# Kernel optimization log

Measured on AMD Instinct MI355X. Metric: run time of the kernel, lower is better.

The kernel has to match this reference:

```python
import jax, jax.numpy as jnp
import numpy as np
from math import sqrt

D_MODEL = 1024
N_HEADS = 16
FFN = 4096
B, N = 2, 2048
EPS = 1e-5


def _layernorm(x, g, b):
    mu = jnp.mean(x, -1, keepdims=True)
    var = jnp.mean((x - mu) ** 2, -1, keepdims=True)
    return (x - mu) * jax.lax.rsqrt(var + EPS) * g + b


def setup_inputs() -> dict:
    key = jax.random.key(0)
    ks = jax.random.split(key, 12)
    s = 1.0 / sqrt(D_MODEL)
    sf = 1.0 / sqrt(FFN)
    inp = {
        "tgt": jax.random.normal(ks[0], (B, N, D_MODEL), jnp.float32),
        # True = masked. Causal: query i may attend to keys j <= i.
        "tgt_mask": jnp.triu(jnp.ones((N, N), jnp.bool_), k=1),
        "tgt_key_pad_mask": jnp.zeros((B, N), jnp.bool_),
        "Wq": jax.random.uniform(ks[1], (D_MODEL, D_MODEL), jnp.float32, -s, s),
        "Wk": jax.random.uniform(ks[2], (D_MODEL, D_MODEL), jnp.float32, -s, s),
        "Wv": jax.random.uniform(ks[3], (D_MODEL, D_MODEL), jnp.float32, -s, s),
        "Wo": jax.random.uniform(ks[4], (D_MODEL, D_MODEL), jnp.float32, -s, s),
        "bo": jax.random.uniform(ks[5], (D_MODEL,), jnp.float32, -s, s),
        "W1": jax.random.uniform(ks[6], (FFN, D_MODEL), jnp.float32, -s, s),
        "b1": jax.random.uniform(ks[7], (FFN,), jnp.float32, -s, s),
        "W2": jax.random.uniform(ks[8], (D_MODEL, FFN), jnp.float32, -sf, sf),
        "b2": jax.random.uniform(ks[9], (D_MODEL,), jnp.float32, -sf, sf),
        "g1": jnp.ones((D_MODEL,), jnp.float32),
        "beta1": jnp.zeros((D_MODEL,), jnp.float32),
        "g2": jnp.ones((D_MODEL,), jnp.float32),
        "beta2": jnp.zeros((D_MODEL,), jnp.float32),
    }
    return inp


def _mha(x, tgt_mask, pad_mask, Wq, Wk, Wv, Wo, bo):
    b, n, d = x.shape
    dk = d // N_HEADS
    q = (x @ Wq.T).reshape(b, n, N_HEADS, dk).transpose(0, 2, 1, 3)  # bhnd
    k = (x @ Wk.T).reshape(b, n, N_HEADS, dk).transpose(0, 2, 1, 3)
    v = (x @ Wv.T).reshape(b, n, N_HEADS, dk).transpose(0, 2, 1, 3)
    scores = jnp.einsum("bhqd,bhkd->bhqk", q, k) / sqrt(dk)
    mask = tgt_mask[None, None, :, :] | pad_mask[:, None, None, :]
    scores = jnp.where(mask, -jnp.inf, scores)
    att = jax.nn.softmax(scores, axis=-1)
    out = jnp.einsum("bhqk,bhkd->bhqd", att, v).transpose(0, 2, 1, 3).reshape(b, n, d)
    return out @ Wo.T + bo


def reference(tgt, tgt_mask, tgt_key_pad_mask, Wq, Wk, Wv, Wo, bo,
              W1, b1, W2, b2, g1, beta1, g2, beta2):
    # PostNorm logic (pre_norm=False), dropout=0 (eval)
    h = _mha(tgt, tgt_mask, tgt_key_pad_mask, Wq, Wk, Wv, Wo, bo)
    x = _layernorm(tgt + h, g1, beta1)
    m = jax.nn.gelu(x @ W1.T + b1, approximate=True) @ W2.T + b2
    return _layernorm(x + m, g2, beta2)
```

## Files before the change

### kernel.cpp

```cpp
#include <hip/hip_runtime.h>


#define DEV __device__ __forceinline__

typedef __attribute__((ext_vector_type(4)))  float f32x4;
typedef __attribute__((ext_vector_type(16))) float f32x16;
typedef __attribute__((ext_vector_type(8)))  short s16x8;

static constexpr int Bb   = 2;
static constexpr int NN   = 2048;
static constexpr int DM   = 1024;
static constexpr int HH   = 16;
static constexpr int DK   = 64;
static constexpr int FF   = 4096;
static constexpr int ROWS = Bb * NN;

#define AS1(p) ((const __attribute__((address_space(1))) void*)(p))
#define AS3(p) ((__attribute__((address_space(3))) void*)(p))

DEV unsigned short f2bf(float f) {
  unsigned u = __float_as_uint(f);
  u += 0x7fff + ((u >> 16) & 1);
  return (unsigned short)(u >> 16);
}
DEV float fexp2(float x) {
  float r;
  asm("v_exp_f32 %0, %1" : "=v"(r) : "v"(x));
  return r;
}
DEV unsigned cvtpk(float lo, float hi) {
  unsigned r;
  asm("v_cvt_pk_bf16_f32 %0, %1, %2" : "=v"(r) : "v"(lo), "v"(hi));
  return r;
}

__global__ __launch_bounds__(256) void k_cast7(
    const float* __restrict__ tgt, const float* __restrict__ Wq,
    const float* __restrict__ Wk, const float* __restrict__ Wv,
    const float* __restrict__ Wo, const float* __restrict__ W1,
    const float* __restrict__ W2,
    ushort* __restrict__ xb, ushort* __restrict__ wqb,
    ushort* __restrict__ w1b, ushort* __restrict__ w2b) {
  const int i = blockIdx.x * 256 + threadIdx.x;
  constexpr int S0 = 1048576;
  constexpr int S1 = 262144;
  const float4* src;
  ushort* dstp;
  if (i < S0)               { src = (const float4*)tgt + i;            dstp = xb  + (size_t)i * 4; }
  else if (i < S0 + S1)     { src = (const float4*)Wq + (i - S0);      dstp = wqb + (size_t)(i - S0) * 4; }
  else if (i < S0 + 2 * S1) { src = (const float4*)Wk + (i - S0 - S1); dstp = wqb + (size_t)(i - S0) * 4; }
  else if (i < S0 + 3 * S1) { src = (const float4*)Wv + (i - S0 - 2 * S1); dstp = wqb + (size_t)(i - S0) * 4; }
  else if (i < S0 + 4 * S1) { src = (const float4*)Wo + (i - S0 - 3 * S1); dstp = wqb + (size_t)(i - S0) * 4; }
  else if (i < 3 * S0)      { src = (const float4*)W1 + (i - 2 * S0);  dstp = w1b + (size_t)(i - 2 * S0) * 4; }
  else                      { src = (const float4*)W2 + (i - 3 * S0);  dstp = w2b + (size_t)(i - 3 * S0) * 4; }
  float4 v = *src;
  ushort4 o;
  o.x = f2bf(v.x); o.y = f2bf(v.y); o.z = f2bf(v.z); o.w = f2bf(v.w);
  *reinterpret_cast<ushort4*>(dstp) = o;
}

template <int EPI, int BN, bool QKV>
__global__ __launch_bounds__(256) void k_gemm(
    const ushort* __restrict__ A, const ushort* __restrict__ Bt,
    const float* __restrict__ bias, const float* __restrict__ resid,
    ushort* __restrict__ Cb, float* __restrict__ Cf,
    int K, int nbx) {
  __shared__ ushort As[2][128][32];
  __shared__ ushort Bs[2][BN][32];

  const int t = threadIdx.x;
  const int lane = t & 63, w = t >> 6;
  const int lr = lane & 15, lg = lane >> 4;
  const int lrow = lane >> 2, lc8 = (lane & 3) * 8;

  const int nwg = gridDim.x;
  const int bid = blockIdx.x;
  const int q8 = nwg >> 3, r8 = nwg & 7;
  const int xcd = bid & 7, lin = bid >> 3;
  const int wg = (xcd < r8 ? xcd * (q8 + 1) : r8 * (q8 + 1) + (xcd - r8) * q8) + lin;
  const int band = wg / (4 * nbx);
  const int inn  = wg % (4 * nbx);
  const int by = band * 4 + (inn & 3);
  const int bx = inn >> 2;

  const int bRow = by * 128;
  const int bCol = bx * BN;

  constexpr int NW = BN / 32;
  const int wRow = (w >> 1) * 64, wCol = (w & 1) * (BN / 2);

  const f32x4 zero = {0.f, 0.f, 0.f, 0.f};
  f32x4 acc[4][NW];
#pragma unroll
  for (int m = 0; m < 4; ++m)
#pragma unroll
    for (int n = 0; n < NW; ++n) acc[m][n] = zero;

  auto stage = [&](int buf, int kt) {
#pragma unroll
    for (int i = 0; i < 2; ++i) {
      int rr = w * 32 + i * 16;
      __builtin_amdgcn_global_load_lds(
          AS1(A + (size_t)(bRow + rr + lrow) * K + kt + lc8),
          AS3(&As[buf][rr][0]), 16, 0, 0);
    }
#pragma unroll
    for (int i = 0; i < BN / 64; ++i) {
      int rr = w * (BN / 4) + i * 16;
      __builtin_amdgcn_global_load_lds(
          AS1(Bt + (size_t)(bCol + rr + lrow) * K + kt + lc8),
          AS3(&Bs[buf][rr][0]), 16, 0, 0);
    }
  };

  stage(0, 0);
  const int nk = K / 32;
  for (int tt = 0; tt < nk; ++tt) {
    const int cur = tt & 1;
    __syncthreads();
    if (tt + 1 < nk) stage(cur ^ 1, (tt + 1) * 32);

    s16x8 af[4], bfr[NW];
#pragma unroll
    for (int m = 0; m < 4; ++m)
      af[m] = *reinterpret_cast<const s16x8*>(&As[cur][wRow + m * 16 + lr][lg * 8]);
#pragma unroll
    for (int n = 0; n < NW; ++n)
      bfr[n] = *reinterpret_cast<const s16x8*>(&Bs[cur][wCol + n * 16 + lr][lg * 8]);
#pragma unroll
    for (int m = 0; m < 4; ++m)
#pragma unroll
      for (int n = 0; n < NW; ++n)
        acc[m][n] = __builtin_amdgcn_mfma_f32_16x16x32_bf16(af[m], bfr[n], acc[m][n], 0, 0, 0);
  }

  ushort* CbOut = Cb;
  int colBase = bCol, Ncols = nbx * BN, third = 0;
  if (QKV) {
    third = bCol >> 10;
    CbOut = Cb + (size_t)third * ROWS * DM;
    colBase = bCol & 1023;
    Ncols = DM;
  }
#pragma unroll
  for (int m = 0; m < 4; ++m) {
    int gr = bRow + wRow + m * 16 + lg * 4;
#pragma unroll
    for (int n = 0; n < NW; ++n) {
      int gc = colBase + wCol + n * 16 + lr;
      float bv = (EPI == 1 || EPI == 2) ? bias[gc] : 0.0f;
#pragma unroll
      for (int r = 0; r < 4; ++r) {
        int nr = gr + r;
        float v = acc[m][n][r] + bv;
        if (EPI == 2) {
          size_t idx = (size_t)nr * Ncols + gc;
          Cf[idx] = v + resid[idx];
        } else if (EPI == 1) {
          size_t idx = (size_t)nr * Ncols + gc;
          float u = v + 0.044715f * v * v * v;
          float g = v / (1.0f + __expf(-1.5957691216057308f * u));
          CbOut[idx] = f2bf(g);
        } else {
          int gcs = gc;
          if (QKV && third == 1)
            gcs = (gc & ~63) | ((gc ^ ((nr & 7) << 3)) & 63);
          CbOut[(size_t)nr * Ncols + gcs] = f2bf(v);
        }
      }
    }
  }
}

__global__ __launch_bounds__(256) void k_vt(const ushort* __restrict__ V,
                                            ushort* __restrict__ vT) {
  __shared__ ushort Ls[64][72];
  const int t = threadIdx.x;
  const int n0 = blockIdx.x * 64;
  const int bh = blockIdx.y;
  const int b = bh >> 4, h = bh & 15;
  const int n = t >> 2;
#pragma unroll
  for (int half = 0; half < 2; ++half) {
    int c8 = ((t & 3) + half * 4) * 8;
    int4 v = *reinterpret_cast<const int4*>(
        V + ((size_t)(b * NN + n0 + n)) * DM + h * DK + c8);
    *reinterpret_cast<int4*>(&Ls[n][c8]) = v;
  }
  __syncthreads();
  const int d = t >> 2;
#pragma unroll
  for (int half = 0; half < 2; ++half) {
    int c = (t & 3) + half * 4;
    ushort tmp[8];
#pragma unroll
    for (int j = 0; j < 8; ++j) tmp[j] = Ls[c * 8 + j][d];
    size_t out = ((size_t)bh * DK + d) * NN + n0 + ((c ^ (d & 7)) * 8);
    *reinterpret_cast<int4*>(vT + out) = *reinterpret_cast<const int4*>(tmp);
  }
}

template <int WB>
__global__ __launch_bounds__(256) void k_ln(const float* __restrict__ in,
                                            const float* __restrict__ g,
                                            const float* __restrict__ bta,
                                            float* __restrict__ outf,
                                            ushort* __restrict__ outb) {
  const int row = blockIdx.x;
  const int t = threadIdx.x;
  float4 v = reinterpret_cast<const float4*>(in + (size_t)row * DM)[t];
  float s1 = v.x + v.y + v.z + v.w;
  float s2 = v.x * v.x + v.y * v.y + v.z * v.z + v.w * v.w;
#pragma unroll
  for (int m = 32; m; m >>= 1) {
    s1 += __shfl_xor(s1, m, 64);
    s2 += __shfl_xor(s2, m, 64);
  }
  __shared__ float red[2][4];
  if ((t & 63) == 0) { red[0][t >> 6] = s1; red[1][t >> 6] = s2; }
  __syncthreads();
  s1 = red[0][0] + red[0][1] + red[0][2] + red[0][3];
  s2 = red[1][0] + red[1][1] + red[1][2] + red[1][3];
  const float mu = s1 * (1.0f / DM);
  const float var = s2 * (1.0f / DM) - mu * mu;
  const float rstd = rsqrtf(var + 1e-5f);
  float4 gv = reinterpret_cast<const float4*>(g)[t];
  float4 bv = reinterpret_cast<const float4*>(bta)[t];
  float4 o;
  o.x = (v.x - mu) * rstd * gv.x + bv.x;
  o.y = (v.y - mu) * rstd * gv.y + bv.y;
  o.z = (v.z - mu) * rstd * gv.z + bv.z;
  o.w = (v.w - mu) * rstd * gv.w + bv.w;
  reinterpret_cast<float4*>(outf + (size_t)row * DM)[t] = o;
  if (WB) {
    ushort4 ob;
    ob.x = f2bf(o.x); ob.y = f2bf(o.y); ob.z = f2bf(o.z); ob.w = f2bf(o.w);
    reinterpret_cast<ushort4*>(outb + (size_t)row * DM)[t] = ob;
  }
}

static __device__ const unsigned char SCHED24[24][2] = {
  {15,0},{15,1},{7,2},
  {14,0},{14,1},{13,0},{13,1},{6,2},
  {12,0},{12,1},{11,0},{11,1},{5,2},
  {10,0},{10,1},{9,0},{9,1},{4,2},
  {8,0},{8,1},{3,2},{2,2},{1,2},{0,2}};

__global__ __launch_bounds__(256) void k_attn(const ushort* __restrict__ Q,
                                              const ushort* __restrict__ Kb,
                                              const ushort* __restrict__ vT,
                                              ushort* __restrict__ O,
                                              float* __restrict__ Op,
                                              float* __restrict__ ml) {
  __shared__ ushort Ks[2][64 * 64];
  __shared__ ushort Vs[2][64 * 64];

  const int t = threadIdx.x;
  const int bid = blockIdx.x;
  const int xcd = bid & 7, j = bid >> 3;
  const int head = j / 24, e = j % 24;
  const int qi = SCHED24[e][0], sv = SCHED24[e][1];
  const int bh = xcd * 4 + head;
  const int kt0 = (sv == 1) ? (qi + 1) : 0;
  const int kt1 = (sv == 0) ? (qi + 1) : (2 * qi + 2);

  const int lane = t & 63, wid = t >> 6;
  const int l31 = lane & 31, hi = lane >> 5;
  const int q0w = qi * 128 + wid * 32;
  const size_t qbase = ((size_t)(bh >> 4) * NN) * DM + (bh & 15) * DK;
  const size_t vbase = (size_t)bh * DK * NN;

  const float C = 0.18033688011112043f;

  s16x8 qf[4];
#pragma unroll
  for (int c = 0; c < 4; ++c)
    qf[c] = *reinterpret_cast<const s16x8*>(Q + qbase + (size_t)(q0w + l31) * DM + c * 16 + hi * 8);

  float mrun = -1e30f, lrun = 0.f, negcm = 1e30f;
  f32x16 accO[2];
#pragma unroll
  for (int dt = 0; dt < 2; ++dt)
#pragma unroll
    for (int r = 0; r < 16; ++r) accO[dt][r] = 0.f;

  auto stage = [&](int buf, int kt) {
    const int kk = kt * 64;
#pragma unroll
    for (int i = 0; i < 2; ++i) {
      int row0 = wid * 16 + i * 8;
      __builtin_amdgcn_global_load_lds(
          AS1(Kb + qbase + (size_t)(kk + row0 + (lane >> 3)) * DM + (lane & 7) * 8),
          AS3(&Ks[buf][row0 * 64]), 16, 0, 0);
      __builtin_amdgcn_global_load_lds(
          AS1(vT + vbase + (size_t)(row0 + (lane >> 3)) * NN + kk + (lane & 7) * 8),
          AS3(&Vs[buf][row0 * 64]), 16, 0, 0);
    }
  };

  stage(0, kt0);
  for (int kt = kt0, li = 0; kt < kt1; ++kt, ++li) {
    const int cur = li & 1;
    const int kk = kt * 64;
    __syncthreads();
    if (kt + 1 < kt1) stage(cur ^ 1, kt + 1);

    if (kk <= q0w + 31) {
      const char* KsB = (const char*)Ks[cur];
      const char* VsB = (const char*)Vs[cur];
      const bool diag = (kk + 64 > q0w);
      const int nsub = (kk + 32 <= q0w + 31) ? 2 : 1;

      f32x16 st[2];
      __builtin_amdgcn_s_setprio(1);
#pragma unroll
      for (int sub = 0; sub < 2; ++sub) {
        if (sub >= nsub) break;
#pragma unroll
        for (int r = 0; r < 16; ++r) st[sub][r] = 0.f;
        const int row = sub * 32 + l31;
        const int swz = (row & 7) << 4;
#pragma unroll
        for (int c = 0; c < 4; ++c) {
          s16x8 kf = *reinterpret_cast<const s16x8*>(KsB + row * 128 + ((c * 32 + hi * 16) ^ swz));
          st[sub] = __builtin_amdgcn_mfma_f32_32x32x16_bf16(kf, qf[c], st[sub], 0, 0, 0);
        }
      }
      __builtin_amdgcn_s_setprio(0);

      const int q = q0w + l31;
      float p[32];
#pragma unroll
      for (int sub = 0; sub < 2; ++sub) {
        if (sub >= nsub) break;
#pragma unroll
        for (int r = 0; r < 16; ++r) {
          float v = st[sub][r];
          if (diag) {
            int kl = sub * 32 + (r & 3) + 8 * (r >> 2) + 4 * hi;
            if (kk + kl > q) v = -1e30f;
          }
          p[sub * 16 + r] = v;
        }
      }
      float a[16];
#pragma unroll
      for (int i = 0; i < 16; ++i) a[i] = (nsub == 2) ? fmaxf(p[i], p[i + 16]) : p[i];
#pragma unroll
      for (int s = 8; s; s >>= 1)
#pragma unroll
        for (int i = 0; i < 8; ++i) if (i < s) a[i] = fmaxf(a[i], a[i + s]);
      float rm = fmaxf(a[0], __shfl_xor(a[0], 32, 64));

      if (__any(rm > mrun)) {
        const float mn = fmaxf(mrun, rm);
        const float alpha = fexp2(C * (mrun - mn));
        mrun = mn;
        negcm = -C * mn;
        lrun *= alpha;
#pragma unroll
        for (int dt = 0; dt < 2; ++dt) accO[dt] *= alpha;
      }

#pragma unroll
      for (int sub = 0; sub < 2; ++sub) {
        if (sub >= nsub) break;
#pragma unroll
        for (int i = 0; i < 16; ++i)
          p[sub * 16 + i] = fexp2(fmaf(p[sub * 16 + i], C, negcm));
      }
#pragma unroll
      for (int i = 0; i < 16; ++i) a[i] = (nsub == 2) ? (p[i] + p[i + 16]) : p[i];
#pragma unroll
      for (int s = 8; s; s >>= 1)
#pragma unroll
        for (int i = 0; i < 8; ++i) if (i < s) a[i] += a[i + s];
      lrun += a[0] + __shfl_xor(a[0], 32, 64);

      s16x8 pf[4];
#pragma unroll
      for (int sub = 0; sub < 2; ++sub) {
        if (sub >= nsub) break;
#pragma unroll
        for (int hf = 0; hf < 2; ++hf) {
          const float* pp = &p[sub * 16 + hf * 8];
          unsigned X0 = cvtpk(pp[0], pp[1]);
          unsigned X1 = cvtpk(pp[2], pp[3]);
          unsigned Y0 = cvtpk(pp[4], pp[5]);
          unsigned Y1 = cvtpk(pp[6], pp[7]);
          asm volatile("v_permlane32_swap_b32 %0, %1" : "+v"(X0), "+v"(Y0));
          asm volatile("v_permlane32_swap_b32 %0, %1" : "+v"(X1), "+v"(Y1));
          union { unsigned u[4]; s16x8 v; } uu;
          uu.u[0] = X0; uu.u[1] = X1; uu.u[2] = Y0; uu.u[3] = Y1;
          pf[sub * 2 + hf] = uu.v;
        }
      }

      __builtin_amdgcn_s_setprio(1);
#pragma unroll
      for (int dt = 0; dt < 2; ++dt) {
        const int d = dt * 32 + l31;
        const int vswz = (d & 7) << 4;
#pragma unroll
        for (int kc = 0; kc < 4; ++kc) {
          if (kc >= nsub * 2) break;
          s16x8 vf = *reinterpret_cast<const s16x8*>(VsB + d * 128 + ((kc * 32 + hi * 16) ^ vswz));
          accO[dt] = __builtin_amdgcn_mfma_f32_32x32x16_bf16(vf, pf[kc], accO[dt], 0, 0, 0);
        }
      }
      __builtin_amdgcn_s_setprio(0);
    }
  }

  if (sv == 2) {
    const int q = q0w + l31;
    const float inv = 1.0f / lrun;
#pragma unroll
    for (int dt = 0; dt < 2; ++dt)
#pragma unroll
      for (int rg = 0; rg < 4; ++rg) {
        int d0 = 8 * rg + 4 * hi + 32 * dt;
        ushort4 ov;
        ov.x = f2bf(accO[dt][rg * 4 + 0] * inv);
        ov.y = f2bf(accO[dt][rg * 4 + 1] * inv);
        ov.z = f2bf(accO[dt][rg * 4 + 2] * inv);
        ov.w = f2bf(accO[dt][rg * 4 + 3] * inv);
        *reinterpret_cast<ushort4*>(O + qbase + (size_t)q * DM + d0) = ov;
      }
  } else {
    const int pidx = (bh * 8 + (qi - 8)) * 2 + sv;
    float* op = Op + (size_t)pidx * (128 * 64);
    const int row = wid * 32 + l31;
#pragma unroll
    for (int dt = 0; dt < 2; ++dt)
#pragma unroll
      for (int rg = 0; rg < 4; ++rg) {
        int d0 = 8 * rg + 4 * hi + 32 * dt;
        f32x4 v4 = { accO[dt][rg * 4 + 0], accO[dt][rg * 4 + 1],
                     accO[dt][rg * 4 + 2], accO[dt][rg * 4 + 3] };
        *reinterpret_cast<f32x4*>(op + (size_t)row * 64 + d0) = v4;
      }
    if (hi == 0) {
      ml[(size_t)pidx * 256 + row * 2 + 0] = mrun;
      ml[(size_t)pidx * 256 + row * 2 + 1] = lrun;
    }
  }
}

__global__ __launch_bounds__(256) void k_amerge(const float* __restrict__ Op,
                                                const float* __restrict__ ml,
                                                ushort* __restrict__ O) {
  const int bh = blockIdx.x >> 3, qq = blockIdx.x & 7;
  const int t = threadIdx.x;
  const int row = t >> 1, dh = (t & 1) * 32;
  const float C = 0.18033688011112043f;

  const int p0 = (bh * 8 + qq) * 2;
  const float m0 = ml[(size_t)p0 * 256 + row * 2 + 0];
  const float l0 = ml[(size_t)p0 * 256 + row * 2 + 1];
  const float m1 = ml[(size_t)(p0 + 1) * 256 + row * 2 + 0];
  const float l1 = ml[(size_t)(p0 + 1) * 256 + row * 2 + 1];
  const float M = fmaxf(m0, m1);
  const float s0 = fexp2(C * (m0 - M));
  const float s1 = fexp2(C * (m1 - M));
  const float inv = 1.0f / (l0 * s0 + l1 * s1);

  const float* o0 = Op + (size_t)p0 * (128 * 64) + (size_t)row * 64 + dh;
  const float* o1 = o0 + 128 * 64;
  const int b = bh >> 4, h = bh & 15;
  const int n = (qq + 8) * 128 + row;
  ushort* dst = O + ((size_t)(b * NN + n)) * DM + h * DK + dh;
#pragma unroll
  for (int i = 0; i < 8; ++i) {
    float4 a = reinterpret_cast<const float4*>(o0)[i];
    float4 c = reinterpret_cast<const float4*>(o1)[i];
    ushort4 ov;
    ov.x = f2bf((a.x * s0 + c.x * s1) * inv);
    ov.y = f2bf((a.y * s0 + c.y * s1) * inv);
    ov.z = f2bf((a.z * s0 + c.z * s1) * inv);
    ov.w = f2bf((a.w * s0 + c.w * s1) * inv);
    reinterpret_cast<ushort4*>(dst)[i] = ov;
  }
}

extern "C" void kernel_launch(void* const* d_in, const int* in_sizes, int n_in,
                              void* d_out, int out_size, void* d_ws, size_t ws_size,
                              hipStream_t stream) {
  const float* tgt = (const float*)d_in[0];
  const float* Wq  = (const float*)d_in[3];
  const float* Wk  = (const float*)d_in[4];
  const float* Wv  = (const float*)d_in[5];
  const float* Wo  = (const float*)d_in[6];
  const float* bo  = (const float*)d_in[7];
  const float* W1  = (const float*)d_in[8];
  const float* b1  = (const float*)d_in[9];
  const float* W2  = (const float*)d_in[10];
  const float* b2  = (const float*)d_in[11];
  const float* g1  = (const float*)d_in[12];
  const float* be1 = (const float*)d_in[13];
  const float* g2  = (const float*)d_in[14];
  const float* be2 = (const float*)d_in[15];

  char* ws = (char*)d_ws;
  size_t off = 0;
  auto alloc = [&](size_t bytes) {
    void* p = ws + off;
    off += (bytes + 255) & ~(size_t)255;
    return p;
  };
  ushort* xb   = (ushort*)alloc((size_t)ROWS * DM * 2);
  ushort* wqb  = (ushort*)alloc((size_t)DM * DM * 2);
  ushort* wkb  = (ushort*)alloc((size_t)DM * DM * 2);
  ushort* wvb  = (ushort*)alloc((size_t)DM * DM * 2);
  ushort* wob  = (ushort*)alloc((size_t)DM * DM * 2);
  ushort* w1b  = (ushort*)alloc((size_t)FF * DM * 2);
  ushort* w2b  = (ushort*)alloc((size_t)DM * FF * 2);
  ushort* qbuf = (ushort*)alloc((size_t)ROWS * DM * 2);
  ushort* kbuf = (ushort*)alloc((size_t)ROWS * DM * 2);
  ushort* vbuf = (ushort*)alloc((size_t)ROWS * DM * 2);
  ushort* vtb  = (ushort*)alloc((size_t)ROWS * DM * 2);
  ushort* atnb = (ushort*)alloc((size_t)ROWS * DM * 2);
  float*  h1   = (float*)alloc((size_t)ROWS * DM * 4);
  float*  x1f  = (float*)alloc((size_t)ROWS * DM * 4);
  ushort* x1b  = (ushort*)alloc((size_t)ROWS * DM * 2);
  ushort* t1b  = (ushort*)alloc((size_t)ROWS * FF * 2);
  float*  Opb  = (float*)alloc((size_t)512 * 128 * 64 * 4);
  float*  mlb  = (float*)alloc((size_t)512 * 256 * 4);
  (void)ws_size; (void)in_sizes; (void)n_in; (void)out_size;
  (void)wkb; (void)wvb; (void)kbuf;

  dim3 blk(256);
  k_cast7<<<dim3(16384), blk, 0, stream>>>(tgt, Wq, Wk, Wv, Wo, W1, W2,
                                           xb, wqb, w1b, w2b);

  k_gemm<0, 128, true><<<dim3(24 * 32), blk, 0, stream>>>(
      xb, wqb, nullptr, nullptr, qbuf, nullptr, DM, 24);

  k_vt<<<dim3(NN / 64, Bb * HH), blk, 0, stream>>>(vbuf, vtb);

  k_attn<<<dim3(768), blk, 0, stream>>>(qbuf, kbuf, vtb, atnb, Opb, mlb);
  k_amerge<<<dim3(256), blk, 0, stream>>>(Opb, mlb, atnb);

  k_gemm<2, 64, false><<<dim3(16 * 32), blk, 0, stream>>>(
      atnb, wob, bo, tgt, nullptr, h1, DM, 16);
  k_ln<1><<<dim3(ROWS), blk, 0, stream>>>(h1, g1, be1, x1f, x1b);

  k_gemm<1, 128, false><<<dim3(32 * 32), blk, 0, stream>>>(
      x1b, w1b, b1, nullptr, t1b, nullptr, DM, 32);
  float* z = h1;
  k_gemm<2, 64, false><<<dim3(16 * 32), blk, 0, stream>>>(
      t1b, w2b, b2, x1f, nullptr, z, FF, 16);
  k_ln<0><<<dim3(ROWS), blk, 0, stream>>>(z, g2, be2, (float*)d_out, nullptr);
}
```

Baseline: 281.6 us.

## Triple-buffer GEMM loads and split-K the FFN down-projection into layernorm

New measurement: 272.2 us. 1.03x faster.

```diff
diff --git a/kernel.cpp b/kernel.cpp
--- a/kernel.cpp
+++ b/kernel.cpp
@@ -59,14 +59,14 @@
   *reinterpret_cast<ushort4*>(dstp) = o;
 }
 
-template <int EPI, int BN, bool QKV>
+template <int EPI, int BN, bool QKV, int SPLITK>
 __global__ __launch_bounds__(256) void k_gemm(
     const ushort* __restrict__ A, const ushort* __restrict__ Bt,
     const float* __restrict__ bias, const float* __restrict__ resid,
     ushort* __restrict__ Cb, float* __restrict__ Cf,
     int K, int nbx) {
-  __shared__ ushort As[2][128][32];
-  __shared__ ushort Bs[2][BN][32];
+  __shared__ ushort As[3][128][32];
+  __shared__ ushort Bs[3][BN][32];
 
   const int t = threadIdx.x;
   const int lane = t & 63, w = t >> 6;
@@ -77,7 +77,9 @@
   const int bid = blockIdx.x;
   const int q8 = nwg >> 3, r8 = nwg & 7;
   const int xcd = bid & 7, lin = bid >> 3;
-  const int wg = (xcd < r8 ? xcd * (q8 + 1) : r8 * (q8 + 1) + (xcd - r8) * q8) + lin;
+  int wg = (xcd < r8 ? xcd * (q8 + 1) : r8 * (q8 + 1) + (xcd - r8) * q8) + lin;
+  int kc = 0;
+  if constexpr (SPLITK == 2) { kc = wg & 1; wg >>= 1; }
   const int band = wg / (4 * nbx);
   const int inn  = wg % (4 * nbx);
   const int by = band * 4 + (inn & 3);
@@ -85,6 +87,9 @@
 
   const int bRow = by * 128;
   const int bCol = bx * BN;
+  const int Kc = K / SPLITK;
+  const int kofs = kc * Kc;
+  const int nk = Kc / 32;
 
   constexpr int NW = BN / 32;
   const int wRow = (w >> 1) * 64, wCol = (w & 1) * (BN / 2);
@@ -96,29 +101,40 @@
 #pragma unroll
     for (int n = 0; n < NW; ++n) acc[m][n] = zero;
 
-  auto stage = [&](int buf, int kt) {
+  auto stage = [&](int buf, int tile) {
+    const int kb = kofs + tile * 32;
 #pragma unroll
     for (int i = 0; i < 2; ++i) {
       int rr = w * 32 + i * 16;
       __builtin_amdgcn_global_load_lds(
-          AS1(A + (size_t)(bRow + rr + lrow) * K + kt + lc8),
+          AS1(A + (size_t)(bRow + rr + lrow) * K + kb + lc8),
           AS3(&As[buf][rr][0]), 16, 0, 0);
     }
 #pragma unroll
     for (int i = 0; i < BN / 64; ++i) {
       int rr = w * (BN / 4) + i * 16;
       __builtin_amdgcn_global_load_lds(
-          AS1(Bt + (size_t)(bCol + rr + lrow) * K + kt + lc8),
+          AS1(Bt + (size_t)(bCol + rr + lrow) * K + kb + lc8),
           AS3(&Bs[buf][rr][0]), 16, 0, 0);
     }
   };
 
   stage(0, 0);
-  const int nk = K / 32;
+  stage(1, 1);
   for (int tt = 0; tt < nk; ++tt) {
-    const int cur = tt & 1;
-    __syncthreads();
-    if (tt + 1 < nk) stage(cur ^ 1, (tt + 1) * 32);
+    const int cur = tt % 3;
+    if (tt + 2 < nk) {
+      stage((tt + 2) % 3, tt + 2);
+      if constexpr (BN == 128) asm volatile("s_waitcnt vmcnt(8)" ::: "memory");
+      else                     asm volatile("s_waitcnt vmcnt(6)" ::: "memory");
+    } else if (tt + 1 < nk) {
+      if constexpr (BN == 128) asm volatile("s_waitcnt vmcnt(4)" ::: "memory");
+      else                     asm volatile("s_waitcnt vmcnt(3)" ::: "memory");
+    } else {
+      asm volatile("s_waitcnt vmcnt(0)" ::: "memory");
+    }
+    __builtin_amdgcn_s_barrier();
+    __builtin_amdgcn_sched_barrier(0);
 
     s16x8 af[4], bfr[NW];
 #pragma unroll
@@ -132,6 +148,10 @@
 #pragma unroll
       for (int n = 0; n < NW; ++n)
         acc[m][n] = __builtin_amdgcn_mfma_f32_16x16x32_bf16(af[m], bfr[n], acc[m][n], 0, 0, 0);
+
+    asm volatile("s_waitcnt lgkmcnt(0)" ::: "memory");
+    __builtin_amdgcn_s_barrier();
+    __builtin_amdgcn_sched_barrier(0);
   }
 
   ushort* CbOut = Cb;
@@ -153,7 +173,9 @@
       for (int r = 0; r < 4; ++r) {
         int nr = gr + r;
         float v = acc[m][n][r] + bv;
-        if (EPI == 2) {
+        if (EPI == 3) {
+          Cf[((size_t)kc * ROWS + nr) * Ncols + gc] = v;
+        } else if (EPI == 2) {
           size_t idx = (size_t)nr * Ncols + gc;
           Cf[idx] = v + resid[idx];
         } else if (EPI == 1) {
@@ -200,8 +222,11 @@
   }
 }
 
-template <int WB>
+template <int WB, int RED>
 __global__ __launch_bounds__(256) void k_ln(const float* __restrict__ in,
+                                            const float* __restrict__ p0,
+                                            const float* __restrict__ p1,
+                                            const float* __restrict__ pb,
                                             const float* __restrict__ g,
                                             const float* __restrict__ bta,
                                             float* __restrict__ outf,
@@ -209,6 +234,15 @@
   const int row = blockIdx.x;
   const int t = threadIdx.x;
   float4 v = reinterpret_cast<const float4*>(in + (size_t)row * DM)[t];
+  if (RED) {
+    float4 a = reinterpret_cast<const float4*>(p0 + (size_t)row * DM)[t];
+    float4 b = reinterpret_cast<const float4*>(p1 + (size_t)row * DM)[t];
+    float4 c = reinterpret_cast<const float4*>(pb)[t];
+    v.x += a.x + b.x + c.x;
+    v.y += a.y + b.y + c.y;
+    v.z += a.z + b.z + c.z;
+    v.w += a.w + b.w + c.w;
+  }
   float s1 = v.x + v.y + v.z + v.w;
   float s2 = v.x * v.x + v.y * v.y + v.z * v.z + v.w * v.w;
 #pragma unroll
@@ -526,6 +560,7 @@
   ushort* t1b  = (ushort*)alloc((size_t)ROWS * FF * 2);
   float*  Opb  = (float*)alloc((size_t)512 * 128 * 64 * 4);
   float*  mlb  = (float*)alloc((size_t)512 * 256 * 4);
+  float*  pp   = (float*)qbuf;
   (void)ws_size; (void)in_sizes; (void)n_in; (void)out_size;
   (void)wkb; (void)wvb; (void)kbuf;
 
@@ -533,7 +568,7 @@
   k_cast7<<<dim3(16384), blk, 0, stream>>>(tgt, Wq, Wk, Wv, Wo, W1, W2,
                                            xb, wqb, w1b, w2b);
 
-  k_gemm<0, 128, true><<<dim3(24 * 32), blk, 0, stream>>>(
+  k_gemm<0, 128, true, 1><<<dim3(24 * 32), blk, 0, stream>>>(
       xb, wqb, nullptr, nullptr, qbuf, nullptr, DM, 24);
 
   k_vt<<<dim3(NN / 64, Bb * HH), blk, 0, stream>>>(vbuf, vtb);
@@ -541,14 +576,15 @@
   k_attn<<<dim3(768), blk, 0, stream>>>(qbuf, kbuf, vtb, atnb, Opb, mlb);
   k_amerge<<<dim3(256), blk, 0, stream>>>(Opb, mlb, atnb);
 
-  k_gemm<2, 64, false><<<dim3(16 * 32), blk, 0, stream>>>(
+  k_gemm<2, 64, false, 1><<<dim3(16 * 32), blk, 0, stream>>>(
       atnb, wob, bo, tgt, nullptr, h1, DM, 16);
-  k_ln<1><<<dim3(ROWS), blk, 0, stream>>>(h1, g1, be1, x1f, x1b);
-
-  k_gemm<1, 128, false><<<dim3(32 * 32), blk, 0, stream>>>(
+  k_ln<1, 0><<<dim3(ROWS), blk, 0, stream>>>(h1, nullptr, nullptr, nullptr,
+                                             g1, be1, x1f, x1b);
+
+  k_gemm<1, 128, false, 1><<<dim3(32 * 32), blk, 0, stream>>>(
       x1b, w1b, b1, nullptr, t1b, nullptr, DM, 32);
-  float* z = h1;
-  k_gemm<2, 64, false><<<dim3(16 * 32), blk, 0, stream>>>(
-      t1b, w2b, b2, x1f, nullptr, z, FF, 16);
-  k_ln<0><<<dim3(ROWS), blk, 0, stream>>>(z, g2, be2, (float*)d_out, nullptr);
-}
+  k_gemm<3, 64, false, 2><<<dim3(2 * 16 * 32), blk, 0, stream>>>(
+      t1b, w2b, nullptr, nullptr, nullptr, pp, FF, 16);
+  k_ln<0, 1><<<dim3(ROWS), blk, 0, stream>>>(x1f, pp, pp + (size_t)ROWS * DM, b2,
+                                             g2, be2, (float*)d_out, nullptr);
+}
```
